# Kernel tuning notes

Measured on AMD Instinct MI355X. Metric: run time of the kernel, lower is better.

The kernel has to match this reference:

```python
import jax, jax.numpy as jnp
import numpy as np

H = 512   # hidden_size
E = 256   # embedding_size
V = 32000 # vocab_size
L = 1024  # max_length (encoder seq len)
B = 64    # batch


def setup_inputs() -> dict:
    key = jax.random.key(0)
    ks = jax.random.split(key, 18)
    n = lambda i, shape, s=0.05: (jax.random.normal(ks[i], shape, dtype=jnp.float32) * s)
    return {
        "input": jax.random.randint(ks[0], (B, 1), 0, V),
        "last_output_context": n(1, (1, B, H), 1.0),
        "last_hidden": n(2, (1, B, H), 1.0),
        "last_cell_state": n(3, (1, B, H), 1.0),
        "encoder_outputs": n(4, (L, B, H), 1.0),
        "emb": n(5, (V, E)),
        "W_ih": n(6, (4 * H, E + H)),
        "W_hh": n(7, (4 * H, H)),
        "b_ih": n(8, (4 * H,)),
        "b_hh": n(9, (4 * H,)),
        "W_attn": n(10, (H, 2 * H)),
        "b_attn": n(11, (H,)),
        "beta": n(12, (H, 1), 1.0),
        "W_oc": n(13, (H, 2 * H)),
        "b_oc": n(14, (H,)),
        "W_out": n(15, (V, H)),
        "b_out": n(16, (V,)),
    }


def reference(input, last_output_context, last_hidden, last_cell_state,
              encoder_outputs, emb, W_ih, W_hh, b_ih, b_hh,
              W_attn, b_attn, beta, W_oc, b_oc, W_out, b_out):
    # embedding lookup: (B,1) -> (B,E)  (permute(1,0,2) then squeeze step dim)
    tok = emb[input[:, 0]]                                   # (B, E)
    x = jnp.concatenate([tok, last_output_context[0]], axis=1)  # (B, E+H)
    # single-step LSTM (PyTorch gate order i, f, g, o)
    gates = x @ W_ih.T + last_hidden[0] @ W_hh.T + b_ih + b_hh  # (B, 4H)
    i_g, f_g, g_g, o_g = jnp.split(gates, 4, axis=1)
    i_g = jax.nn.sigmoid(i_g)
    f_g = jax.nn.sigmoid(f_g)
    g_g = jnp.tanh(g_g)
    o_g = jax.nn.sigmoid(o_g)
    c = f_g * last_cell_state[0] + i_g * g_g                  # (B, H)
    h = o_g * jnp.tanh(c)                                     # (B, H) == rnn_output
    # additive attention, vectorized over the seq_len loop
    h_tiled = jnp.broadcast_to(h[None], (L, B, H))
    cat = jnp.concatenate([h_tiled, encoder_outputs], axis=-1)  # (L, B, 2H)
    energy = jnp.tanh(cat @ W_attn.T + b_attn) @ beta           # (L, B, 1)
    attn_w = jax.nn.softmax(energy[..., 0], axis=0)             # (L, B) softmax over seq
    # context = bmm(attn_weights, encoder_outputs)
    context = jnp.einsum('lb,lbh->bh', attn_w, encoder_outputs)  # (B, H)
    co = jnp.tanh(jnp.concatenate([h, context], axis=1) @ W_oc.T + b_oc)  # (B, H)
    output = jax.nn.log_softmax(co @ W_out.T + b_out, axis=1)    # (B, V)
    return output, co[None], h[None], c[None]
```

## Files before the change

### kernel.cpp

```cpp
#include <hip/hip_runtime.h>
#include <hip/hip_bf16.h>
#include <cstddef>

#define H   512
#define E   256
#define V   32000
#define L   1024
#define B   64
#define KX  768
#define M_TOT 65536

typedef __attribute__((ext_vector_type(8))) _Float16 half8v;
typedef __attribute__((ext_vector_type(4))) float f32x4;

__device__ __forceinline__ half8v cvt8(float4 x0, float4 x1) {
    union { half8v v; _Float16 u[8]; } hv;
    hv.u[0] = (_Float16)x0.x; hv.u[1] = (_Float16)x0.y;
    hv.u[2] = (_Float16)x0.z; hv.u[3] = (_Float16)x0.w;
    hv.u[4] = (_Float16)x1.x; hv.u[5] = (_Float16)x1.y;
    hv.u[6] = (_Float16)x1.z; hv.u[7] = (_Float16)x1.w;
    return hv.v;
}

__global__ __launch_bounds__(256) void k_conv_w(const float* __restrict__ W_attn,
                                                unsigned short* __restrict__ Wf) {
    int e0 = blockIdx.x * 2048 + threadIdx.x * 8;
    int j = e0 >> 9, k = e0 & 511;
    const float* src = &W_attn[(size_t)j * (2 * H) + H + k];
    float4 x0 = *reinterpret_cast<const float4*>(src);
    float4 x1 = *reinterpret_cast<const float4*>(src + 4);
    half8v hv = cvt8(x0, x1);
    *reinterpret_cast<half8v*>(&Wf[e0]) = hv;
}

__global__ __launch_bounds__(256) void k_build(const int* __restrict__ inp,
                                               const float* __restrict__ loc,
                                               const float* __restrict__ hprev,
                                               const float* __restrict__ emb,
                                               float* __restrict__ xprevT) {
    int gid = blockIdx.x * 256 + threadIdx.x;
    int k = gid >> 6, b = gid & 63;
    float v;
    if (k < 256)      v = emb[(size_t)inp[b] * E + k];
    else if (k < 768) v = loc[b * H + (k - 256)];
    else              v = hprev[b * H + (k - 768)];
    xprevT[gid] = v;
}

__global__ __launch_bounds__(256) void k_lstm(const float* __restrict__ W_ih,
                                              const float* __restrict__ W_hh,
                                              const float* __restrict__ b_ih,
                                              const float* __restrict__ b_hh,
                                              const float* __restrict__ xprevT,
                                              const float* __restrict__ cprev,
                                              float* __restrict__ h_out,
                                              float* __restrict__ c_out,
                                              float* __restrict__ hnewT) {
    int u = blockIdx.x;
    int w = threadIdx.x >> 6;
    int b = threadIdx.x & 63;
    int j = w * 512 + u;
    float a0 = 0.f, a1 = 0.f, a2 = 0.f, a3 = 0.f;
    const float* Wr = &W_ih[(size_t)j * KX];
    for (int k = 0; k < KX; k += 4) {
        float4 wv = *reinterpret_cast<const float4*>(&Wr[k]);
        a0 += wv.x * xprevT[(k + 0) * 64 + b];
        a1 += wv.y * xprevT[(k + 1) * 64 + b];
        a2 += wv.z * xprevT[(k + 2) * 64 + b];
        a3 += wv.w * xprevT[(k + 3) * 64 + b];
    }
    const float* Wr2 = &W_hh[(size_t)j * H];
    const float* hT = &xprevT[KX * 64];
    for (int k = 0; k < H; k += 4) {
        float4 wv = *reinterpret_cast<const float4*>(&Wr2[k]);
        a0 += wv.x * hT[(k + 0) * 64 + b];
        a1 += wv.y * hT[(k + 1) * 64 + b];
        a2 += wv.z * hT[(k + 2) * 64 + b];
        a3 += wv.w * hT[(k + 3) * 64 + b];
    }
    float acc = b_ih[j] + b_hh[j] + ((a0 + a1) + (a2 + a3));
    __shared__ float gs[4][64];
    gs[w][b] = acc;
    __syncthreads();
    if (threadIdx.x < 64) {
        float ig = 1.f / (1.f + __expf(-gs[0][b]));
        float fg = 1.f / (1.f + __expf(-gs[1][b]));
        float gg = tanhf(gs[2][b]);
        float og = 1.f / (1.f + __expf(-gs[3][b]));
        float c = fg * cprev[b * H + u] + ig * gg;
        float h = og * tanhf(c);
        c_out[b * H + u] = c;
        h_out[b * H + u] = h;
        hnewT[u * 64 + b] = h;
    }
}

__global__ __launch_bounds__(256) void k_hw(const float* __restrict__ W_attn,
                                            const float* __restrict__ b_attn,
                                            const float* __restrict__ hT,
                                            float* __restrict__ hW_jb) {
    int j = blockIdx.x * 4 + (threadIdx.x >> 6);
    int b = threadIdx.x & 63;
    float a0 = 0.f, a1 = 0.f, a2 = 0.f, a3 = 0.f;
    const float* Wr = &W_attn[(size_t)j * (2 * H)];
    for (int k = 0; k < H; k += 4) {
        float4 wv = *reinterpret_cast<const float4*>(&Wr[k]);
        a0 += wv.x * hT[(k + 0) * 64 + b];
        a1 += wv.y * hT[(k + 1) * 64 + b];
        a2 += wv.z * hT[(k + 2) * 64 + b];
        a3 += wv.w * hT[(k + 3) * 64 + b];
    }
    hW_jb[j * 64 + b] = b_attn[j] + ((a0 + a1) + (a2 + a3));
}

#define EPITCH 520

__global__ __launch_bounds__(256, 2) void k_energy_v6(
        const float* __restrict__ enc,
        const unsigned short* __restrict__ Wf,
        const float* __restrict__ hW,
        const float* __restrict__ beta,
        float* __restrict__ energy) {
    __shared__ unsigned short As[64 * EPITCH];
    __shared__ float red[4][64];

    const int tid  = threadIdx.x;
    const int lane = tid & 63;
    const int w    = tid >> 6;
    const int m0   = blockIdx.x * 64;

    {
        int row = tid >> 2;
        int kbase = (tid & 3) * 128;
        const float* src = &enc[(size_t)(m0 + row) * H + kbase];
        #pragma unroll
        for (int c = 0; c < 16; ++c) {
            float4 x0 = *reinterpret_cast<const float4*>(src + c * 8);
            float4 x1 = *reinterpret_cast<const float4*>(src + c * 8 + 4);
            half8v hv = cvt8(x0, x1);
            *reinterpret_cast<half8v*>(&As[row * EPITCH + kbase + c * 8]) = hv;
        }
    }
    __syncthreads();

    const int fr = lane & 15;
    const int kb = (lane >> 4) * 8;

    f32x4 acc[4][8];
    #pragma unroll
    for (int mf = 0; mf < 4; ++mf)
        #pragma unroll
        for (int nf = 0; nf < 8; ++nf) acc[mf][nf] = (f32x4){0.f, 0.f, 0.f, 0.f};

    const unsigned short* Bbase = &Wf[(size_t)(w * 128 + fr) * H + kb];

    for (int k0 = 0; k0 < H; k0 += 32) {
        half8v a_h[4];
        #pragma unroll
        for (int mf = 0; mf < 4; ++mf)
            a_h[mf] = *reinterpret_cast<const half8v*>(
                &As[(mf * 16 + fr) * EPITCH + k0 + kb]);
        #pragma unroll
        for (int nf = 0; nf < 8; ++nf) {
            half8v b_h = *reinterpret_cast<const half8v*>(&Bbase[(size_t)nf * 16 * H + k0]);
            #pragma unroll
            for (int mf = 0; mf < 4; ++mf)
                acc[mf][nf] = __builtin_amdgcn_mfma_f32_16x16x32_f16(
                    a_h[mf], b_h, acc[mf][nf], 0, 0, 0);
        }
    }

    float psum[4][4];
    #pragma unroll
    for (int i = 0; i < 4; ++i)
        #pragma unroll
        for (int r = 0; r < 4; ++r) psum[i][r] = 0.f;
    #pragma unroll
    for (int nf = 0; nf < 8; ++nf) {
        int jj = w * 128 + nf * 16 + fr;
        float bet = beta[jj];
        #pragma unroll
        for (int mf = 0; mf < 4; ++mf) {
            int b_base = mf * 16 + (lane >> 4) * 4;
            float4 hw4 = *reinterpret_cast<const float4*>(&hW[jj * 64 + b_base]);
            float hwv[4] = {hw4.x, hw4.y, hw4.z, hw4.w};
            #pragma unroll
            for (int r = 0; r < 4; ++r) {
                float e = acc[mf][nf][r] + hwv[r];
                float ex = __expf(2.f * e);
                psum[mf][r] += bet * (1.f - 2.f / (ex + 1.f));
            }
        }
    }
    #pragma unroll
    for (int mf = 0; mf < 4; ++mf)
        #pragma unroll
        for (int r = 0; r < 4; ++r) {
            float v = psum[mf][r];
            v += __shfl_xor(v, 1);
            v += __shfl_xor(v, 2);
            v += __shfl_xor(v, 4);
            v += __shfl_xor(v, 8);
            psum[mf][r] = v;
        }
    if (fr == 0) {
        #pragma unroll
        for (int mf = 0; mf < 4; ++mf)
            #pragma unroll
            for (int r = 0; r < 4; ++r)
                red[w][mf * 16 + (lane >> 4) * 4 + r] = psum[mf][r];
    }
    __syncthreads();
    if (tid < 64)
        energy[m0 + tid] = (red[0][tid] + red[1][tid]) + (red[2][tid] + red[3][tid]);
}

__global__ __launch_bounds__(256) void k_softmax_l(const float* __restrict__ energy,
                                                   float* __restrict__ attn_w) {
    int b = blockIdx.x;
    int tid = threadIdx.x;
    float el[4];
    float m = -1e30f;
    #pragma unroll
    for (int i = 0; i < 4; ++i) {
        int l = i * 256 + tid;
        float e = energy[l * 64 + b];
        el[i] = e;
        m = fmaxf(m, e);
    }
    #pragma unroll
    for (int s = 1; s < 64; s <<= 1) m = fmaxf(m, __shfl_xor(m, s));
    __shared__ float redm[4];
    if ((tid & 63) == 0) redm[tid >> 6] = m;
    __syncthreads();
    m = fmaxf(fmaxf(redm[0], redm[1]), fmaxf(redm[2], redm[3]));
    float s = 0.f;
    #pragma unroll
    for (int i = 0; i < 4; ++i) { el[i] = __expf(el[i] - m); s += el[i]; }
    #pragma unroll
    for (int sh = 1; sh < 64; sh <<= 1) s += __shfl_xor(s, sh);
    __shared__ float reds[4];
    if ((tid & 63) == 0) reds[tid >> 6] = s;
    __syncthreads();
    s = reds[0] + reds[1] + reds[2] + reds[3];
    float inv = 1.f / s;
    #pragma unroll
    for (int i = 0; i < 4; ++i)
        attn_w[(i * 256 + tid) * 64 + b] = el[i] * inv;
}

__global__ __launch_bounds__(128) void k_ctx_part(const float* __restrict__ attn_w,
                                                  const float* __restrict__ enc,
                                                  float* __restrict__ ctx_part) {
    int chunk = blockIdx.x, b = blockIdx.y;
    int h = threadIdx.x * 4;
    float4 acc = {0.f, 0.f, 0.f, 0.f};
    for (int i = 0; i < 32; ++i) {
        int l = chunk * 32 + i;
        float w = attn_w[l * 64 + b];
        float4 e4 = *reinterpret_cast<const float4*>(
            &enc[((size_t)l * 64 + b) * H + h]);
        acc.x += w * e4.x;
        acc.y += w * e4.y;
        acc.z += w * e4.z;
        acc.w += w * e4.w;
    }
    *reinterpret_cast<float4*>(&ctx_part[((size_t)(chunk * 64 + b)) * H + h]) = acc;
}

__global__ __launch_bounds__(256) void k_ctx_reduce(const float* __restrict__ ctx_part,
                                                    float* __restrict__ ctxT) {
    int gid = blockIdx.x * 256 + threadIdx.x;
    int b = gid >> 9, h = gid & 511;
    float s = 0.f;
    for (int c = 0; c < 32; ++c)
        s += ctx_part[((size_t)(c * 64 + b)) * H + h];
    ctxT[h * 64 + b] = s;
}

__global__ __launch_bounds__(256) void k_co(const float* __restrict__ W_oc,
                                            const float* __restrict__ b_oc,
                                            const float* __restrict__ hT,
                                            const float* __restrict__ ctxT,
                                            float* __restrict__ co_out) {
    int j = blockIdx.x * 4 + (threadIdx.x >> 6);
    int b = threadIdx.x & 63;
    float a0 = 0.f, a1 = 0.f, a2 = 0.f, a3 = 0.f;
    const float* Wr = &W_oc[(size_t)j * (2 * H)];
    for (int k = 0; k < H; k += 4) {
        float4 wv = *reinterpret_cast<const float4*>(&Wr[k]);
        a0 += wv.x * hT[(k + 0) * 64 + b];
        a1 += wv.y * hT[(k + 1) * 64 + b];
        a2 += wv.z * hT[(k + 2) * 64 + b];
        a3 += wv.w * hT[(k + 3) * 64 + b];
    }
    const float* Wr2 = Wr + H;
    for (int k = 0; k < H; k += 4) {
        float4 wv = *reinterpret_cast<const float4*>(&Wr2[k]);
        a0 += wv.x * ctxT[(k + 0) * 64 + b];
        a1 += wv.y * ctxT[(k + 1) * 64 + b];
        a2 += wv.z * ctxT[(k + 2) * 64 + b];
        a3 += wv.w * ctxT[(k + 3) * 64 + b];
    }
    co_out[b * H + j] = tanhf(b_oc[j] + ((a0 + a1) + (a2 + a3)));
}

__global__ __launch_bounds__(256) void k_logits_v3(const float* __restrict__ co,
                                                   const float* __restrict__ W_out,
                                                   const float* __restrict__ b_out,
                                                   float* __restrict__ logits) {
    const int tid  = threadIdx.x;
    const int lane = tid & 63;
    const int w    = tid >> 6;
    const int fr   = lane & 15;
    const int kb   = (lane >> 4) * 8;
    const int j    = blockIdx.x * 64 + w * 16 + fr;

    f32x4 acc[4];
    #pragma unroll
    for (int mf = 0; mf < 4; ++mf) acc[mf] = (f32x4){0.f, 0.f, 0.f, 0.f};

    const float* Arow = &co[(size_t)fr * H + kb];
    const float* Brow = &W_out[(size_t)j * H + kb];

    for (int k0 = 0; k0 < H; k0 += 32) {
        float4 b0 = *reinterpret_cast<const float4*>(Brow + k0);
        float4 b1 = *reinterpret_cast<const float4*>(Brow + k0 + 4);
        half8v bh = cvt8(b0, b1);
        #pragma unroll
        for (int mf = 0; mf < 4; ++mf) {
            const float* ap = Arow + (size_t)mf * 16 * H + k0;
            float4 a0 = *reinterpret_cast<const float4*>(ap);
            float4 a1 = *reinterpret_cast<const float4*>(ap + 4);
            half8v ah = cvt8(a0, a1);
            acc[mf] = __builtin_amdgcn_mfma_f32_16x16x32_f16(ah, bh, acc[mf], 0, 0, 0);
        }
    }
    float bo = b_out[j];
    #pragma unroll
    for (int mf = 0; mf < 4; ++mf) {
        int mbase = mf * 16 + (lane >> 4) * 4;
        #pragma unroll
        for (int r = 0; r < 4; ++r)
            logits[(size_t)(mbase + r) * V + j] = acc[mf][r] + bo;
    }
}

__global__ __launch_bounds__(256) void k_lsm_part(const float* __restrict__ logits,
                                                  float* __restrict__ pmax,
                                                  float* __restrict__ psum) {
    int chunk = blockIdx.x, b = blockIdx.y;
    int tid = threadIdx.x;
    const float* row = &logits[(size_t)b * V + chunk * 4000];
    float v[16];
    float m = -1e30f;
    #pragma unroll
    for (int t = 0; t < 16; ++t) {
        int i = t * 256 + tid;
        v[t] = (i < 4000) ? row[i] : -1e30f;
        m = fmaxf(m, v[t]);
    }
    #pragma unroll
    for (int s = 1; s < 64; s <<= 1) m = fmaxf(m, __shfl_xor(m, s));
    __shared__ float redm[4];
    if ((tid & 63) == 0) redm[tid >> 6] = m;
    __syncthreads();
    m = fmaxf(fmaxf(redm[0], redm[1]), fmaxf(redm[2], redm[3]));
    float s = 0.f;
    #pragma unroll
    for (int t = 0; t < 16; ++t) s += __expf(v[t] - m);
    #pragma unroll
    for (int sh = 1; sh < 64; sh <<= 1) s += __shfl_xor(s, sh);
    __shared__ float reds[4];
    if ((tid & 63) == 0) reds[tid >> 6] = s;
    __syncthreads();
    if (tid == 0) {
        pmax[chunk * 64 + b] = m;
        psum[chunk * 64 + b] = reds[0] + reds[1] + reds[2] + reds[3];
    }
}

__global__ __launch_bounds__(64) void k_lsm_final(const float* __restrict__ pmax,
                                                  const float* __restrict__ psum,
                                                  float* __restrict__ lse) {
    int b = threadIdx.x;
    float m = -1e30f;
    #pragma unroll
    for (int c = 0; c < 8; ++c) m = fmaxf(m, pmax[c * 64 + b]);
    float s = 0.f;
    #pragma unroll
    for (int c = 0; c < 8; ++c) s += psum[c * 64 + b] * __expf(pmax[c * 64 + b] - m);
    lse[b] = m + __logf(s);
}

__global__ __launch_bounds__(256) void k_lsm_write(const float* __restrict__ logits,
                                                   const float* __restrict__ lse,
                                                   float* __restrict__ out) {
    size_t i4 = ((size_t)blockIdx.x * 256 + threadIdx.x) * 4;
    int b = (int)(i4 / V);
    float l = lse[b];
    float4 x = *reinterpret_cast<const float4*>(&logits[i4]);
    x.x -= l; x.y -= l; x.z -= l; x.w -= l;
    *reinterpret_cast<float4*>(&out[i4]) = x;
}

extern "C" void kernel_launch(void* const* d_in, const int* in_sizes, int n_in,
                              void* d_out, int out_size, void* d_ws, size_t ws_size,
                              hipStream_t stream) {
    const int*   inp    = (const int*)  d_in[0];
    const float* loc    = (const float*)d_in[1];
    const float* hprev  = (const float*)d_in[2];
    const float* cprev  = (const float*)d_in[3];
    const float* enc    = (const float*)d_in[4];
    const float* emb    = (const float*)d_in[5];
    const float* W_ih   = (const float*)d_in[6];
    const float* W_hh   = (const float*)d_in[7];
    const float* b_ih   = (const float*)d_in[8];
    const float* b_hh   = (const float*)d_in[9];
    const float* W_attn = (const float*)d_in[10];
    const float* b_attn = (const float*)d_in[11];
    const float* beta   = (const float*)d_in[12];
    const float* W_oc   = (const float*)d_in[13];
    const float* b_oc   = (const float*)d_in[14];
    const float* W_out  = (const float*)d_in[15];
    const float* b_out  = (const float*)d_in[16];

    float* out = (float*)d_out;
    float* out_co = out + (size_t)B * V;
    float* out_h  = out_co + B * H;
    float* out_c  = out_h  + B * H;

    float* ws = (float*)d_ws;
    float* xprevT = ws;
    float* hnewT  = xprevT + 1280 * 64;
    float* hW     = hnewT  + H * 64;
    float* energy = hW     + H * 64;
    float* attnw  = energy + M_TOT;
    float* ctxp   = attnw  + M_TOT;
    float* ctxT   = ctxp   + 32 * 64 * H;
    float* logits = ctxT   + H * 64;
    float* pmax   = logits + (size_t)B * V;
    float* psum   = pmax   + 512;
    float* lse    = psum   + 512;
    unsigned short* Wf = (unsigned short*)(lse + 64);

    k_conv_w<<<128, 256, 0, stream>>>(W_attn, Wf);
    k_build <<<320, 256, 0, stream>>>(inp, loc, hprev, emb, xprevT);
    k_lstm  <<<512, 256, 0, stream>>>(W_ih, W_hh, b_ih, b_hh, xprevT, cprev,
                                      out_h, out_c, hnewT);
    k_hw    <<<128, 256, 0, stream>>>(W_attn, b_attn, hnewT, hW);
    k_energy_v6<<<1024, 256, 0, stream>>>(enc, Wf, hW, beta, energy);
    k_softmax_l<<<64, 256, 0, stream>>>(energy, attnw);
    k_ctx_part <<<dim3(32, 64), 128, 0, stream>>>(attnw, enc, ctxp);
    k_ctx_reduce<<<128, 256, 0, stream>>>(ctxp, ctxT);
    k_co    <<<128, 256, 0, stream>>>(W_oc, b_oc, hnewT, ctxT, out_co);
    k_logits_v3<<<500, 256, 0, stream>>>(out_co, W_out, b_out, logits);
    k_lsm_part<<<dim3(8, 64), 256, 0, stream>>>(logits, pmax, psum);
    k_lsm_final<<<1, 64, 0, stream>>>(pmax, psum, lse);
    k_lsm_write<<<2000, 256, 0, stream>>>(logits, lse, out);
}
```

Baseline: 313.2 us.

## Retile energy GEMM into 128x128 K-looped tiles with register prefetch and XCD mapping

Replaces the energy kernel, which staged a full 64x512 enc tile in LDS and read W from global memory, with a classic 128x128 output tile that streams K in 32-wide slices through small LDS buffers. The next slice is prefetched into registers while the current one is computed. Block IDs are swizzled so each XCD handles a contiguous group of M tiles. The J dimension is split into four tiles that write partial energies, which the softmax kernel now sums. This should raise occupancy and B reuse, at the cost of reading enc four times (once per J tile) and writing a 4x larger partial buffer.

```diff
diff --git a/kernel.cpp b/kernel.cpp
--- a/kernel.cpp
+++ b/kernel.cpp
@@ -113,75 +113,105 @@
     hW_jb[j * 64 + b] = b_attn[j] + ((a0 + a1) + (a2 + a3));
 }
 
-#define EPITCH 520
-
-__global__ __launch_bounds__(256, 2) void k_energy_v6(
+#define BKE 32
+#define PITCH 40
+
+__global__ __launch_bounds__(256, 4) void k_energy_v7(
         const float* __restrict__ enc,
         const unsigned short* __restrict__ Wf,
         const float* __restrict__ hW,
         const float* __restrict__ beta,
-        float* __restrict__ energy) {
-    __shared__ unsigned short As[64 * EPITCH];
-    __shared__ float red[4][64];
+        float* __restrict__ partial_e) {
+    __shared__ unsigned short Ah[128 * PITCH];
+    __shared__ unsigned short Bh[128 * PITCH];
+    __shared__ float red[2][128];
 
     const int tid  = threadIdx.x;
     const int lane = tid & 63;
-    const int w    = tid >> 6;
-    const int m0   = blockIdx.x * 64;
-
-    {
-        int row = tid >> 2;
-        int kbase = (tid & 3) * 128;
-        const float* src = &enc[(size_t)(m0 + row) * H + kbase];
-        #pragma unroll
-        for (int c = 0; c < 16; ++c) {
-            float4 x0 = *reinterpret_cast<const float4*>(src + c * 8);
-            float4 x1 = *reinterpret_cast<const float4*>(src + c * 8 + 4);
-            half8v hv = cvt8(x0, x1);
-            *reinterpret_cast<half8v*>(&As[row * EPITCH + kbase + c * 8]) = hv;
-        }
-    }
-    __syncthreads();
-
-    const int fr = lane & 15;
-    const int kb = (lane >> 4) * 8;
-
-    f32x4 acc[4][8];
-    #pragma unroll
-    for (int mf = 0; mf < 4; ++mf)
-        #pragma unroll
-        for (int nf = 0; nf < 8; ++nf) acc[mf][nf] = (f32x4){0.f, 0.f, 0.f, 0.f};
-
-    const unsigned short* Bbase = &Wf[(size_t)(w * 128 + fr) * H + kb];
-
-    for (int k0 = 0; k0 < H; k0 += 32) {
-        half8v a_h[4];
+    const int wave = tid >> 6;
+    const int wm = wave >> 1;
+    const int wn = wave & 1;
+    const int bid = blockIdx.x;
+    const int xcd = bid & 7;
+    const int loc = bid >> 3;
+    const int mt  = xcd * 64 + (loc >> 2);
+    const int jt  = loc & 3;
+    const int m0 = mt * 128;
+    const int j0 = jt * 128;
+
+    const int srow = tid >> 2;
+    const int skc  = tid & 3;
+
+    float4 ra0[2], ra1[2];
+    half8v rb[2];
+    #pragma unroll
+    for (int p = 0; p < 2; ++p) {
+        int row = p * 64 + srow;
+        const float* asrc = &enc[(size_t)(m0 + row) * H + skc * 8];
+        ra0[p] = *reinterpret_cast<const float4*>(asrc);
+        ra1[p] = *reinterpret_cast<const float4*>(asrc + 4);
+        rb[p] = *reinterpret_cast<const half8v*>(&Wf[(size_t)(j0 + row) * H + skc * 8]);
+    }
+
+    f32x4 acc[4][4];
+    #pragma unroll
+    for (int i = 0; i < 4; ++i)
+        #pragma unroll
+        for (int j = 0; j < 4; ++j) acc[i][j] = (f32x4){0.f, 0.f, 0.f, 0.f};
+
+    for (int k0 = 0; k0 < H; k0 += BKE) {
+        __syncthreads();
+        #pragma unroll
+        for (int p = 0; p < 2; ++p) {
+            half8v hv = cvt8(ra0[p], ra1[p]);
+            int off = (p * 64 + srow) * PITCH + skc * 8;
+            *reinterpret_cast<half8v*>(&Ah[off]) = hv;
+            *reinterpret_cast<half8v*>(&Bh[off]) = rb[p];
+        }
+        __syncthreads();
+        if (k0 + BKE < H) {
+            int kn = k0 + BKE;
+            #pragma unroll
+            for (int p = 0; p < 2; ++p) {
+                int row = p * 64 + srow;
+                const float* asrc = &enc[(size_t)(m0 + row) * H + kn + skc * 8];
+                ra0[p] = *reinterpret_cast<const float4*>(asrc);
+                ra1[p] = *reinterpret_cast<const float4*>(asrc + 4);
+                rb[p] = *reinterpret_cast<const half8v*>(&Wf[(size_t)(j0 + row) * H + kn + skc * 8]);
+            }
+        }
+        const int fr = lane & 15;
+        const int kb = (lane >> 4) * 8;
+        half8v a_h[4], b_h[4];
+        #pragma unroll
+        for (int mf = 0; mf < 4; ++mf) {
+            int off = (wm * 64 + mf * 16 + fr) * PITCH + kb;
+            a_h[mf] = *reinterpret_cast<const half8v*>(&Ah[off]);
+        }
+        #pragma unroll
+        for (int nf = 0; nf < 4; ++nf) {
+            int off = (wn * 64 + nf * 16 + fr) * PITCH + kb;
+            b_h[nf] = *reinterpret_cast<const half8v*>(&Bh[off]);
+        }
         #pragma unroll
         for (int mf = 0; mf < 4; ++mf)
-            a_h[mf] = *reinterpret_cast<const half8v*>(
-                &As[(mf * 16 + fr) * EPITCH + k0 + kb]);
-        #pragma unroll
-        for (int nf = 0; nf < 8; ++nf) {
-            half8v b_h = *reinterpret_cast<const half8v*>(&Bbase[(size_t)nf * 16 * H + k0]);
             #pragma unroll
-            for (int mf = 0; mf < 4; ++mf)
+            for (int nf = 0; nf < 4; ++nf)
                 acc[mf][nf] = __builtin_amdgcn_mfma_f32_16x16x32_f16(
-                    a_h[mf], b_h, acc[mf][nf], 0, 0, 0);
-        }
-    }
-
+                    a_h[mf], b_h[nf], acc[mf][nf], 0, 0, 0);
+    }
     float psum[4][4];
     #pragma unroll
     for (int i = 0; i < 4; ++i)
         #pragma unroll
         for (int r = 0; r < 4; ++r) psum[i][r] = 0.f;
     #pragma unroll
-    for (int nf = 0; nf < 8; ++nf) {
-        int jj = w * 128 + nf * 16 + fr;
+    for (int nf = 0; nf < 4; ++nf) {
+        int jj = j0 + wn * 64 + nf * 16 + (lane & 15);
         float bet = beta[jj];
         #pragma unroll
         for (int mf = 0; mf < 4; ++mf) {
-            int b_base = mf * 16 + (lane >> 4) * 4;
+            int b_base = (wm * 64 + mf * 16 + (lane >> 4) * 4) & 63;
             float4 hw4 = *reinterpret_cast<const float4*>(&hW[jj * 64 + b_base]);
             float hwv[4] = {hw4.x, hw4.y, hw4.z, hw4.w};
             #pragma unroll
@@ -203,19 +233,20 @@
             v += __shfl_xor(v, 8);
             psum[mf][r] = v;
         }
-    if (fr == 0) {
+    __syncthreads();
+    if ((lane & 15) == 0) {
         #pragma unroll
         for (int mf = 0; mf < 4; ++mf)
             #pragma unroll
             for (int r = 0; r < 4; ++r)
-                red[w][mf * 16 + (lane >> 4) * 4 + r] = psum[mf][r];
-    }
-    __syncthreads();
-    if (tid < 64)
-        energy[m0 + tid] = (red[0][tid] + red[1][tid]) + (red[2][tid] + red[3][tid]);
-}
-
-__global__ __launch_bounds__(256) void k_softmax_l(const float* __restrict__ energy,
+                red[wn][wm * 64 + mf * 16 + (lane >> 4) * 4 + r] = psum[mf][r];
+    }
+    __syncthreads();
+    if (tid < 128)
+        partial_e[(size_t)jt * M_TOT + m0 + tid] = red[0][tid] + red[1][tid];
+}
+
+__global__ __launch_bounds__(256) void k_softmax_l(const float* __restrict__ partial_e,
                                                    float* __restrict__ attn_w) {
     int b = blockIdx.x;
     int tid = threadIdx.x;
@@ -224,7 +255,10 @@
     #pragma unroll
     for (int i = 0; i < 4; ++i) {
         int l = i * 256 + tid;
-        float e = energy[l * 64 + b];
+        float e = 0.f;
+        #pragma unroll
+        for (int nb = 0; nb < 4; ++nb)
+            e += partial_e[(size_t)nb * M_TOT + l * 64 + b];
         el[i] = e;
         m = fmaxf(m, e);
     }
@@ -434,8 +468,8 @@
     float* xprevT = ws;
     float* hnewT  = xprevT + 1280 * 64;
     float* hW     = hnewT  + H * 64;
-    float* energy = hW     + H * 64;
-    float* attnw  = energy + M_TOT;
+    float* pe     = hW     + H * 64;
+    float* attnw  = pe     + 4 * M_TOT;
     float* ctxp   = attnw  + M_TOT;
     float* ctxT   = ctxp   + 32 * 64 * H;
     float* logits = ctxT   + H * 64;
@@ -449,8 +483,8 @@
     k_lstm  <<<512, 256, 0, stream>>>(W_ih, W_hh, b_ih, b_hh, xprevT, cprev,
                                       out_h, out_c, hnewT);
     k_hw    <<<128, 256, 0, stream>>>(W_attn, b_attn, hnewT, hW);
-    k_energy_v6<<<1024, 256, 0, stream>>>(enc, Wf, hW, beta, energy);
-    k_softmax_l<<<64, 256, 0, stream>>>(energy, attnw);
+    k_energy_v7<<<2048, 256, 0, stream>>>(enc, Wf, hW, beta, pe);
+    k_softmax_l<<<64, 256, 0, stream>>>(pe, attnw);
     k_ctx_part <<<dim3(32, 64), 128, 0, stream>>>(attnw, enc, ctxp);
     k_ctx_reduce<<<128, 256, 0, stream>>>(ctxp, ctxT);
     k_co    <<<128, 256, 0, stream>>>(W_oc, b_oc, hnewT, ctxT, out_co);
```

New measurement: 254.8 us. 1.23x faster.
